# Performance work log

Hardware: AMD Instinct MI355X
Metric: run time of the kernel (lower is better)

Reference implementation:

```python
import jax, jax.numpy as jnp
import numpy as np

N_NODES = 50000
N_G_EDGES = 400000
N_LG_EDGES = 600000
N_HEADS = 4
OUT_FEATS = 64
EPS = 0.001


def segment_mean(x, seg_ids, num_segments):
    s = jax.ops.segment_sum(x, seg_ids, num_segments=num_segments)
    cnt = jax.ops.segment_sum(jnp.ones((x.shape[0],), x.dtype), seg_ids, num_segments=num_segments)
    return s / jnp.maximum(cnt, 1.0)[(...,) + (None,) * (x.ndim - 1)]


def setup_inputs() -> dict:
    key = jax.random.key(0)
    ks = jax.random.split(key, 12)
    return {
        'atomic_number': jax.random.randint(ks[0], (N_NODES,), 0, 4),
        'g_src': jax.random.randint(ks[1], (N_G_EDGES,), 0, N_NODES),
        'g_dst': jax.random.randint(ks[2], (N_G_EDGES,), 0, N_NODES),
        'lg_src': jax.random.randint(ks[3], (N_LG_EDGES,), 0, N_G_EDGES),
        'lg_dst': jax.random.randint(ks[4], (N_LG_EDGES,), 0, N_G_EDGES),
        'costheta': jax.random.uniform(ks[5], (N_LG_EDGES,), jnp.float32),
        'dnr': jax.random.uniform(ks[6], (N_LG_EDGES,), jnp.float32),
        'a': jax.random.uniform(ks[7], (N_HEADS,), jnp.float32),
        'b': jax.random.uniform(ks[8], (N_HEADS,), jnp.float32),
        'c': jax.random.uniform(ks[9], (N_HEADS,), jnp.float32),
        'd': jax.random.uniform(ks[10], (N_HEADS,), jnp.float32),
        'value_table': jax.random.normal(ks[11], (4, OUT_FEATS * N_HEADS), jnp.float32),
    }


def reference(atomic_number, g_src, g_dst, lg_src, lg_dst, costheta, dnr, a, b, c, d, value_table):
    # send_k_src: per g-edge atomic numbers of endpoints
    k_src = atomic_number[g_src]  # (E_g,)
    k_dst = atomic_number[g_dst]  # (E_g,)

    # masked symmetry key on line-graph edges (edge pair: lg_src -> lg_dst, g-edge indices)
    ka = k_src[lg_src]
    kc = k_dst[lg_dst]
    kb = k_dst[lg_src]
    peripheral = (ka == kc).astype(jnp.int32)
    central = ((kb == ka) & (kb == kc)).astype(jnp.int32)
    sym_key = peripheral * 2 + central  # (E_lg,), values in {0,1,2,3}

    # value embedding lookup -> (E_lg, F, H)
    asv = value_table[sym_key].reshape(N_LG_EDGES, OUT_FEATS, N_HEADS)

    # angular / radial symmetry per head
    ct = jnp.clip(costheta, -EPS, EPS)
    theta = jnp.arccos(ct)[:, None]  # (E_lg, 1)
    B = b % jnp.pi
    angular = ((jnp.cos(a[None, :] * theta + B[None, :]) + 1.0) / 2.0) ** c[None, :]  # (E_lg, H)
    radial = jnp.exp(-d[None, :] * (dnr[:, None] ** 2))  # (E_lg, H)
    spatial = radial * angular

    sv = asv * spatial[:, None, :]  # (E_lg, F, H)

    # reverse line-graph mean: aggregate lg edges by their (original) source lg-node = g-edge
    w_edge = segment_mean(sv, lg_src, N_G_EDGES)  # (E_g, F, H)
    # reverse graph mean: aggregate g edges by their (original) source node
    w_node = segment_mean(w_edge, g_src, N_NODES)  # (N, F, H)

    return jnp.sum(w_node, axis=-1)  # (N, F)
```

## Files before the change

### kernel.cpp

```cpp
#include <hip/hip_runtime.h>
#include <math.h>

typedef unsigned long long u64;
typedef unsigned int u32;
typedef unsigned short u16;
typedef unsigned char u8;

#define N_NODES    50000
#define N_G_EDGES  400000
#define N_LG_EDGES 600000
#define OUT_FEATS  64
#define EPSV       0.001f
#define PI_F       3.14159265358979323846f
#define HPI_F      1.57079632679489662f
#define FXSCALE    512.0f
#define INV_FXSCALE (1.0f/512.0f)

#define CT_SCALE   3.2e7f
#define CT_INV     (1.0f/3.2e7f)
#define DN_SCALE   65535.0f
#define DN_INV     (1.0f/65535.0f)

#define SB_N    256
#define EPB1    2344
#define GH_B0   256
#define GH_N    16
#define GH_EPC  25000
#define GH_W    12500
#define PK_B0   272
#define PK_GPB  3572
#define K1_GRID 384

#define WID   1564
#define NPB   196
#define SPB   (NPB*4)
#define CAP2  2816


__global__ __launch_bounds__(1024) void k1(const int* __restrict__ an,
                                           const int* __restrict__ gsrc,
                                           const int* __restrict__ gdst,
                                           const int* __restrict__ lgsrc,
                                           const int* __restrict__ lgdst,
                                           const float* __restrict__ costheta,
                                           const float* __restrict__ dnr,
                                           u8*  __restrict__ kk8,
                                           u32* __restrict__ cg,
                                           u32* __restrict__ prefT1,
                                           u64* __restrict__ sme64) {
    __shared__ u64 sm64[6250];
    const int tid = threadIdx.x;
    const int bid = blockIdx.x;

    if (bid < SB_N) {
        u64* metaS = sm64;
        u32* lcnt  = (u32*)(sm64 + 2344);
        u32* pref  = (u32*)(sm64 + 2344) + 256;
        if (tid < 256) lcnt[tid] = 0u;
        __syncthreads();

        const int e0 = bid * EPB1;
        const int e1 = (e0 + EPB1 < N_LG_EDGES) ? e0 + EPB1 : N_LG_EDGES;
        u64 pv[3]; u32 mv[3];
#pragma unroll
        for (int it = 0; it < 3; ++it) {
            mv[it] = 0u;
            int e = e0 + it * 1024 + tid;
            if (e < e1) {
                int ls = __builtin_nontemporal_load(&lgsrc[e]);
                int ld = __builtin_nontemporal_load(&lgdst[e]);
                float ct = __builtin_nontemporal_load(&costheta[e]);
                float dn = __builtin_nontemporal_load(&dnr[e]);
                float cc = fminf(fmaxf(ct, -EPSV), EPSV);
                u32 ct16 = (u32)(u16)(cc * CT_SCALE + 32768.0f + 0.5f);
                float dns = dn * DN_SCALE + 0.5f;
                u32 dn16 = (u32)(dns < 65535.0f ? (u16)dns : (u16)65535u);
                u32 bk = (u32)ls / WID;
                u32 li = (u32)ls - bk * WID;
                pv[it] = (u64)li | ((u64)(u32)ld << 11) | ((u64)dn16 << 30)
                       | ((u64)ct16 << 46);
                u32 rank = atomicAdd(&lcnt[bk], 1u);
                mv[it] = 0x80000000u | (rank << 8) | bk;
            }
        }
        __syncthreads();
        if (tid < 256) pref[tid + 1] = lcnt[tid];
        if (tid == 0) pref[0] = 0u;
        __syncthreads();
        for (int off = 1; off < 256; off <<= 1) {
            u32 add = 0;
            if (tid < 256 && tid >= off) add = pref[tid - off + 1];
            __syncthreads();
            if (tid < 256) pref[tid + 1] += add;
            __syncthreads();
        }
#pragma unroll
        for (int it = 0; it < 3; ++it) {
            if (mv[it] & 0x80000000u) {
                u32 bk = mv[it] & 0xffu;
                u32 pos = pref[bk] + ((mv[it] >> 8) & 0x7fffffu);
                metaS[pos] = pv[it];
            }
        }
        __syncthreads();
        const u32 btot = pref[256];
        for (u32 i = tid; i < btot; i += 1024)
            __builtin_nontemporal_store(metaS[i], &sme64[(size_t)bid * EPB1 + i]);
        if (tid <= 256) prefT1[bid * 257 + tid] = pref[tid];
    } else if (bid < PK_B0) {
        u32* hist = (u32*)sm64;
        const int cc = bid - GH_B0;
        for (int w = tid; w < GH_W; w += 1024) hist[w] = 0u;
        __syncthreads();
        const int s0 = cc * GH_EPC;
        for (int g = s0 + tid; g < s0 + GH_EPC; g += 1024) {
            int n = gsrc[g];
            atomicAdd(&hist[n >> 2], 1u << (8 * (n & 3)));
        }
        __syncthreads();
        for (int w = tid; w < GH_W; w += 1024) cg[cc * GH_W + w] = hist[w];
    } else {
        const int g0 = (bid - PK_B0) * PK_GPB;
        const int g1 = (g0 + PK_GPB < N_G_EDGES) ? g0 + PK_GPB : N_G_EDGES;
        for (int g = g0 + tid; g < g1; g += 1024)
            kk8[g] = (u8)(an[gsrc[g]] | (an[gdst[g]] << 4));
    }
}

__global__ __launch_bounds__(1024) void k2(const int* __restrict__ gsrc,
                                           const u8*  __restrict__ kk8,
                                           const u32* __restrict__ prefT1,
                                           const u64* __restrict__ sme64,
                                           const float* __restrict__ pa,
                                           const float* __restrict__ pb,
                                           const float* __restrict__ pc,
                                           const float* __restrict__ pd,
                                           u64* __restrict__ mq64,
                                           u32* __restrict__ prefT2) {
    __shared__ u64 sm64[5632 + 78];
    __shared__ u32 su[4154];
    u64* stage  = sm64;
    u64* outst  = sm64 + 2816;
    u32* cntinv = su;
    u32* nkw    = su + 1564;
    u32* sstart = su + 3128;
    u32* soff   = su + 3384;
    u32* lcnt2  = su + 3641;
    u32* pref2  = su + 3897;
    const int tid = threadIdx.x;
    const int b = blockIdx.x;
    const int lo = b * WID;

    for (int i = tid; i < WID; i += 1024) cntinv[i] = 0u;
    if (tid < 256) {
        u32 a = prefT1[tid * 257 + b];
        u32 c2 = prefT1[tid * 257 + b + 1];
        sstart[tid] = a; soff[tid + 1] = c2 - a; lcnt2[tid] = 0u;
    }
    if (tid == 0) soff[0] = 0u;
    __syncthreads();
    for (int off = 1; off < 256; off <<= 1) {
        u32 add = 0;
        if (tid < 256 && tid >= off) add = soff[tid - off + 1];
        __syncthreads();
        if (tid < 256) soff[tid + 1] += add;
        __syncthreads();
    }
    u32 total = soff[256]; if (total > CAP2) total = CAP2;

    {
        const int g = tid >> 2, lane = tid & 3;
        const u32 st = sstart[g];
        const u32 base = soff[g];
        const u32 len = soff[g + 1] - base;
        const u64* src = sme64 + (size_t)g * EPB1 + st;
        for (u32 j = lane; j < len; j += 4) {
            u32 p = base + j;
            if (p < CAP2) stage[p] = __builtin_nontemporal_load(&src[j]);
        }
    }
    for (int i = tid; i < WID; i += 1024) {
        int ls = lo + i;
        u32 nk = 0u;
        if (ls < N_G_EDGES)
            nk = (u32)(u16)gsrc[ls] | ((u32)kk8[ls] << 16);
        nkw[i] = nk;
    }
    __syncthreads();
    for (u32 i = tid; i < total; i += 1024)
        atomicAdd(&cntinv[(u32)(stage[i] & 0x7ffu)], 1u);
    __syncthreads();
    for (int i = tid; i < WID; i += 1024) {
        u32 c = cntinv[i];
        cntinv[i] = __float_as_uint(1.0f / (float)(c < 1u ? 1u : c));
    }
    __syncthreads();

    float A0[4], A1[4], A2[4], DD[4];
#pragma unroll
    for (int h = 0; h < 4; ++h) {
        float a = pa[h], B = fmodf(pb[h], PI_F), c = pc[h], d = pd[h];
        float K = a * HPI_F + B;
        float ck = cosf(K), sk = sinf(K);
        float u0 = 0.5f * (1.0f + ck);
        float f0 = powf(u0, c);
        float g1v = (-0.5f * a * sk) / u0;
        float u2 = -0.25f * a * a * ck;
        float g2v = u2 / u0 - 0.5f * g1v * g1v;
        A0[h] = f0;
        A1[h] = f0 * c * g1v;
        A2[h] = f0 * (c * g2v + 0.5f * c * c * g1v * g1v);
        DD[h] = d;
    }

    u64 qv[3]; u32 mv2[3];
#pragma unroll
    for (int it = 0; it < 3; ++it) {
        mv2[it] = 0u;
        u32 i = (u32)(it * 1024 + tid);
        if (i < total) {
            u64 v = stage[i];
            u32 li = (u32)(v & 0x7ffu);
            u32 ld = (u32)((v >> 11) & 0x7ffffu);
            float dn = (float)(u32)((v >> 30) & 0xffffu) * DN_INV;
            float ct = ((float)(u32)((v >> 46) & 0xffffu) - 32768.0f) * CT_INV;
            float inv = __uint_as_float(cntinv[li]);
            u32 nk = nkw[li];
            int node = (int)(nk & 0xffffu);
            u32 kw = (nk >> 16) & 0xffu;
            int ka = (int)(kw & 0xfu);
            int kb = (int)(kw >> 4);
            int kd = kk8[ld] >> 4;
            int key = ((ka == kd) ? 2 : 0) + ((kb == ka && kb == kd) ? 1 : 0);
            float del = -ct;
            float dn2 = dn * dn;
            float s = inv * FXSCALE;
            u64 q = 0;
#pragma unroll
            for (int h = 0; h < 4; ++h) {
                float ang = A0[h] + del * (A1[h] + del * A2[h]);
                float rad = __expf(-DD[h] * dn2);
                q |= (u64)(u32)(ang * rad * s + 0.5f) << (10 * h);
            }
            u32 nb = (u32)node / NPB;
            u32 slot = ((u32)node - nb * NPB) * 4u + (u32)key;
            u32 rank = atomicAdd(&lcnt2[nb], 1u);
            qv[it] = (q << 10) | (u64)slot;
            mv2[it] = 0x80000000u | (rank << 18) | (nb << 10);
        }
    }
    __syncthreads();
    if (tid < 256) pref2[tid + 1] = lcnt2[tid];
    if (tid == 0) pref2[0] = 0u;
    __syncthreads();
    for (int off = 1; off < 256; off <<= 1) {
        u32 add = 0;
        if (tid < 256 && tid >= off) add = pref2[tid - off + 1];
        __syncthreads();
        if (tid < 256) pref2[tid + 1] += add;
        __syncthreads();
    }
#pragma unroll
    for (int it = 0; it < 3; ++it) {
        if (mv2[it] & 0x80000000u) {
            u32 nb = (mv2[it] >> 10) & 0xffu;
            u32 pos = pref2[nb] + ((mv2[it] >> 18) & 0x1fffu);
            if (pos < CAP2) outst[pos] = qv[it];
        }
    }
    __syncthreads();
    u32 t2 = pref2[256]; if (t2 > CAP2) t2 = CAP2;
    for (u32 i = tid; i < t2; i += 1024)
        __builtin_nontemporal_store(outst[i], &mq64[(size_t)b * CAP2 + i]);
    if (tid <= 256) {
        u32 v = pref2[tid];
        prefT2[b * 257 + tid] = (v < CAP2) ? v : CAP2;
    }
}

__global__ __launch_bounds__(1024) void k3(const u64* __restrict__ mq64,
                                           const u32* __restrict__ prefT2,
                                           const u32* __restrict__ cg,
                                           const float* __restrict__ VT,
                                           float* __restrict__ out) {
    __shared__ u64 sm64[2816 + 784];
    __shared__ u32 su[2506];
    u64* stage  = sm64;
    u64* ts     = sm64 + 2816;
    float* vt_s = (float*)su;
    float* ivg  = (float*)(su + 1024);
    u32* sstart = su + 1220;
    u32* soff   = su + 1476;
    const int tid = threadIdx.x;
    const int nb = blockIdx.x;

    for (int i = tid; i < SPB; i += 1024) ts[i] = 0ull;
    vt_s[tid] = VT[tid];
    if (tid < NPB) {
        int n = nb * NPB + tid;
        float iv = 0.0f;
        if (n < N_NODES) {
            int w = n >> 2, sh = 8 * (n & 3);
            u32 c = 0;
#pragma unroll
            for (int cc = 0; cc < GH_N; ++cc)
                c += (cg[cc * GH_W + w] >> sh) & 0xffu;
            iv = 1.0f / (float)(c < 1u ? 1u : c);
        }
        ivg[tid] = iv;
    }
    if (tid < 256) {
        u32 a = prefT2[tid * 257 + nb];
        u32 c2 = prefT2[tid * 257 + nb + 1];
        sstart[tid] = a; soff[tid + 1] = c2 - a;
    }
    if (tid == 0) soff[0] = 0u;
    __syncthreads();
    for (int off = 1; off < 256; off <<= 1) {
        u32 add = 0;
        if (tid < 256 && tid >= off) add = soff[tid - off + 1];
        __syncthreads();
        if (tid < 256) soff[tid + 1] += add;
        __syncthreads();
    }
    u32 total = soff[256]; if (total > CAP2) total = CAP2;

    {
        const int g = tid >> 2, lane = tid & 3;
        const u32 st = sstart[g];
        const u32 base = soff[g];
        const u32 len = soff[g + 1] - base;
        const u64* src = mq64 + (size_t)g * CAP2 + st;
        for (u32 j = lane; j < len; j += 4) {
            u32 p = base + j;
            if (p < CAP2) stage[p] = __builtin_nontemporal_load(&src[j]);
        }
    }
    __syncthreads();

    for (u32 i = tid; i < total; i += 1024) {
        u64 v = stage[i];
        u32 slot = (u32)(v & 0x3ffu);
        u64 q = ((v >> 10) & 0x3ffu) | (((v >> 20) & 0x3ffu) << 16)
              | (((v >> 30) & 0x3ffu) << 32) | (((v >> 40) & 0x3ffu) << 48);
        atomicAdd(&ts[slot], q);
    }
    __syncthreads();

    const int n0 = nb * NPB;
    for (int j = tid; j < NPB * OUT_FEATS; j += 1024) {
        int nl = j >> 6, f = j & 63;
        int n = n0 + nl;
        if (n < N_NODES) {
            float acc = 0.0f;
#pragma unroll
            for (int k = 0; k < 4; ++k) {
                u64 t = ts[nl * 4 + k];
#pragma unroll
                for (int h = 0; h < 4; ++h) {
                    float tv = (float)((u32)(t >> (16 * h)) & 0xffffu);
                    acc += vt_s[k * 256 + f * 4 + h] * tv;
                }
            }
            __builtin_nontemporal_store(acc * INV_FXSCALE * ivg[nl],
                                        &out[n * OUT_FEATS + f]);
        }
    }
}

extern "C" void kernel_launch(void* const* d_in, const int* in_sizes, int n_in,
                              void* d_out, int out_size, void* d_ws, size_t ws_size,
                              hipStream_t stream) {
    const int*   an       = (const int*)d_in[0];
    const int*   gsrc     = (const int*)d_in[1];
    const int*   gdst     = (const int*)d_in[2];
    const int*   lgsrc    = (const int*)d_in[3];
    const int*   lgdst    = (const int*)d_in[4];
    const float* costheta = (const float*)d_in[5];
    const float* dnr      = (const float*)d_in[6];
    const float* pa       = (const float*)d_in[7];
    const float* pb       = (const float*)d_in[8];
    const float* pc       = (const float*)d_in[9];
    const float* pd       = (const float*)d_in[10];
    const float* vt       = (const float*)d_in[11];
    float* out = (float*)d_out;

    char* ws = (char*)d_ws;
    u8*  kk8    = (u8*) (ws + 0);
    u32* cg     = (u32*)(ws + 400000);
    u32* prefT1 = (u32*)(ws + 1200000);
    u32* prefT2 = (u32*)(ws + 1463168);
    u64* sme64  = (u64*)(ws + 1726336);
    u64* mq64   = (u64*)(ws + 6526848);

    k1<<<dim3(K1_GRID), dim3(1024), 0, stream>>>(
        an, gsrc, gdst, lgsrc, lgdst, costheta, dnr, kk8, cg, prefT1, sme64);
    k2<<<dim3(256), dim3(1024), 0, stream>>>(
        gsrc, kk8, prefT1, sme64, pa, pb, pc, pd, mq64, prefT2);
    k3<<<dim3(256), dim3(1024), 0, stream>>>(
        mq64, prefT2, cg, vt, out);
}
```

Before: 48.51 us.

## Double bucket count to 512 blocks of 512 threads across all three kernels

Re-partitions the three-pass bucketed scatter/reduce pipeline from 256 blocks of 1024 threads to 512 blocks of 512 threads. Bucket widths, capacities and the bit-packing layouts shrink to match. The source-node histogram is also split into range-restricted sub-blocks so each fits in smaller shared memory. The aim is more blocks to fill the 256 CUs and less shared memory per block. In exchange, each block does a longer 512-step prefix scan, the gather loop becomes one serial thread per source segment, and the prefix tables are larger.

```diff
diff --git a/kernel.cpp b/kernel.cpp
--- a/kernel.cpp
+++ b/kernel.cpp
@@ -21,51 +21,54 @@
 #define DN_SCALE   65535.0f
 #define DN_INV     (1.0f/65535.0f)
 
-#define SB_N    256
-#define EPB1    2344
-#define GH_B0   256
-#define GH_N    16
+#define NB    512
+#define NTH   512
+#define WID   782
+#define EPB   1172
+#define CAP3  1536
+#define NPB   98
+#define SPB   (NPB*4)
+
+#define GH_B0   512
+#define GH_CH   16
 #define GH_EPC  25000
-#define GH_W    12500
-#define PK_B0   272
+#define GH_BR   3125
+#define GH_W    782
+#define GH_CSTR 12512
+#define PK_B0   768
 #define PK_GPB  3572
-#define K1_GRID 384
-
-#define WID   1564
-#define NPB   196
-#define SPB   (NPB*4)
-#define CAP2  2816
-
-
-__global__ __launch_bounds__(1024) void k1(const int* __restrict__ an,
-                                           const int* __restrict__ gsrc,
-                                           const int* __restrict__ gdst,
-                                           const int* __restrict__ lgsrc,
-                                           const int* __restrict__ lgdst,
-                                           const float* __restrict__ costheta,
-                                           const float* __restrict__ dnr,
-                                           u8*  __restrict__ kk8,
-                                           u32* __restrict__ cg,
-                                           u32* __restrict__ prefT1,
-                                           u64* __restrict__ sme64) {
-    __shared__ u64 sm64[6250];
+#define K1_GRID 880
+
+
+__global__ __launch_bounds__(NTH) void k1(const int* __restrict__ an,
+                                          const int* __restrict__ gsrc,
+                                          const int* __restrict__ gdst,
+                                          const int* __restrict__ lgsrc,
+                                          const int* __restrict__ lgdst,
+                                          const float* __restrict__ costheta,
+                                          const float* __restrict__ dnr,
+                                          u8*  __restrict__ kk8,
+                                          u32* __restrict__ cg,
+                                          u32* __restrict__ prefT1,
+                                          u64* __restrict__ sme64) {
+    __shared__ u64 stageS[EPB];
+    __shared__ u32 su[1025];
     const int tid = threadIdx.x;
     const int bid = blockIdx.x;
 
-    if (bid < SB_N) {
-        u64* metaS = sm64;
-        u32* lcnt  = (u32*)(sm64 + 2344);
-        u32* pref  = (u32*)(sm64 + 2344) + 256;
-        if (tid < 256) lcnt[tid] = 0u;
-        __syncthreads();
-
-        const int e0 = bid * EPB1;
-        const int e1 = (e0 + EPB1 < N_LG_EDGES) ? e0 + EPB1 : N_LG_EDGES;
+    if (bid < NB) {
+        u32* lcnt = su;
+        u32* pref = su + 512;
+        lcnt[tid] = 0u;
+        __syncthreads();
+
+        const int e0 = bid * EPB;
+        const int e1 = (e0 + EPB < N_LG_EDGES) ? e0 + EPB : N_LG_EDGES;
         u64 pv[3]; u32 mv[3];
 #pragma unroll
         for (int it = 0; it < 3; ++it) {
             mv[it] = 0u;
-            int e = e0 + it * 1024 + tid;
+            int e = e0 + it * NTH + tid;
             if (e < e1) {
                 int ls = __builtin_nontemporal_load(&lgsrc[e]);
                 int ld = __builtin_nontemporal_load(&lgdst[e]);
@@ -77,109 +80,111 @@
                 u32 dn16 = (u32)(dns < 65535.0f ? (u16)dns : (u16)65535u);
                 u32 bk = (u32)ls / WID;
                 u32 li = (u32)ls - bk * WID;
-                pv[it] = (u64)li | ((u64)(u32)ld << 11) | ((u64)dn16 << 30)
-                       | ((u64)ct16 << 46);
+                pv[it] = (u64)li | ((u64)(u32)ld << 10) | ((u64)dn16 << 29)
+                       | ((u64)ct16 << 45);
                 u32 rank = atomicAdd(&lcnt[bk], 1u);
-                mv[it] = 0x80000000u | (rank << 8) | bk;
+                mv[it] = 0x80000000u | (rank << 19) | (bk << 10);
             }
         }
         __syncthreads();
-        if (tid < 256) pref[tid + 1] = lcnt[tid];
+        pref[tid + 1] = lcnt[tid];
         if (tid == 0) pref[0] = 0u;
         __syncthreads();
-        for (int off = 1; off < 256; off <<= 1) {
+        for (int off = 1; off < NB; off <<= 1) {
             u32 add = 0;
-            if (tid < 256 && tid >= off) add = pref[tid - off + 1];
+            if (tid >= off) add = pref[tid - off + 1];
             __syncthreads();
-            if (tid < 256) pref[tid + 1] += add;
+            pref[tid + 1] += add;
             __syncthreads();
         }
 #pragma unroll
         for (int it = 0; it < 3; ++it) {
             if (mv[it] & 0x80000000u) {
-                u32 bk = mv[it] & 0xffu;
-                u32 pos = pref[bk] + ((mv[it] >> 8) & 0x7fffffu);
-                metaS[pos] = pv[it];
+                u32 bk = (mv[it] >> 10) & 0x1ffu;
+                u32 pos = pref[bk] + ((mv[it] >> 19) & 0x7ffu);
+                stageS[pos] = pv[it];
             }
         }
         __syncthreads();
-        const u32 btot = pref[256];
-        for (u32 i = tid; i < btot; i += 1024)
-            __builtin_nontemporal_store(metaS[i], &sme64[(size_t)bid * EPB1 + i]);
-        if (tid <= 256) prefT1[bid * 257 + tid] = pref[tid];
+        const u32 btot = pref[NB];
+        for (u32 i = tid; i < btot; i += NTH)
+            __builtin_nontemporal_store(stageS[i], &sme64[(size_t)bid * EPB + i]);
+        prefT1[bid * 513 + tid] = pref[tid];
+        if (tid == 0) prefT1[bid * 513 + 512] = pref[512];
     } else if (bid < PK_B0) {
-        u32* hist = (u32*)sm64;
-        const int cc = bid - GH_B0;
-        for (int w = tid; w < GH_W; w += 1024) hist[w] = 0u;
+        u32* hist = su;
+        const int b2 = bid - GH_B0;
+        const int cc = b2 & 15, r = b2 >> 4;
+        const int lo = r * GH_BR;
+        for (int w = tid; w < GH_W; w += NTH) hist[w] = 0u;
         __syncthreads();
         const int s0 = cc * GH_EPC;
-        for (int g = s0 + tid; g < s0 + GH_EPC; g += 1024) {
-            int n = gsrc[g];
-            atomicAdd(&hist[n >> 2], 1u << (8 * (n & 3)));
-        }
-        __syncthreads();
-        for (int w = tid; w < GH_W; w += 1024) cg[cc * GH_W + w] = hist[w];
+        for (int g = s0 + tid; g < s0 + GH_EPC; g += NTH) {
+            unsigned lb = (unsigned)(gsrc[g] - lo);
+            if (lb < (unsigned)GH_BR)
+                atomicAdd(&hist[lb >> 2], 1u << (8 * (lb & 3)));
+        }
+        __syncthreads();
+        for (int w = tid; w < GH_W; w += NTH)
+            cg[cc * GH_CSTR + r * GH_W + w] = hist[w];
     } else {
         const int g0 = (bid - PK_B0) * PK_GPB;
         const int g1 = (g0 + PK_GPB < N_G_EDGES) ? g0 + PK_GPB : N_G_EDGES;
-        for (int g = g0 + tid; g < g1; g += 1024)
+        for (int g = g0 + tid; g < g1; g += NTH)
             kk8[g] = (u8)(an[gsrc[g]] | (an[gdst[g]] << 4));
     }
 }
 
-__global__ __launch_bounds__(1024) void k2(const int* __restrict__ gsrc,
-                                           const u8*  __restrict__ kk8,
-                                           const u32* __restrict__ prefT1,
-                                           const u64* __restrict__ sme64,
-                                           const float* __restrict__ pa,
-                                           const float* __restrict__ pb,
-                                           const float* __restrict__ pc,
-                                           const float* __restrict__ pd,
-                                           u64* __restrict__ mq64,
-                                           u32* __restrict__ prefT2) {
-    __shared__ u64 sm64[5632 + 78];
-    __shared__ u32 su[4154];
-    u64* stage  = sm64;
-    u64* outst  = sm64 + 2816;
-    u32* cntinv = su;
-    u32* nkw    = su + 1564;
-    u32* sstart = su + 3128;
-    u32* soff   = su + 3384;
-    u32* lcnt2  = su + 3641;
-    u32* pref2  = su + 3897;
+__global__ __launch_bounds__(NTH) void k2(const int* __restrict__ gsrc,
+                                          const u8*  __restrict__ kk8,
+                                          const u32* __restrict__ prefT1,
+                                          const u64* __restrict__ sme64,
+                                          const float* __restrict__ pa,
+                                          const float* __restrict__ pb,
+                                          const float* __restrict__ pc,
+                                          const float* __restrict__ pd,
+                                          u64* __restrict__ mq64,
+                                          u32* __restrict__ prefT2) {
+    __shared__ u64 stage[CAP3];
+    __shared__ u64 outst[CAP3];
+    __shared__ u32 cntinv[WID];
+    __shared__ u32 nkw[WID];
+    __shared__ u32 sstart[NB];
+    __shared__ u32 soff[NB + 1];
+    __shared__ u32 lcnt2[NB];
+    __shared__ u32 pref2[NB + 1];
     const int tid = threadIdx.x;
     const int b = blockIdx.x;
     const int lo = b * WID;
 
-    for (int i = tid; i < WID; i += 1024) cntinv[i] = 0u;
-    if (tid < 256) {
-        u32 a = prefT1[tid * 257 + b];
-        u32 c2 = prefT1[tid * 257 + b + 1];
+    for (int i = tid; i < WID; i += NTH) cntinv[i] = 0u;
+    {
+        u32 a = prefT1[tid * 513 + b];
+        u32 c2 = prefT1[tid * 513 + b + 1];
         sstart[tid] = a; soff[tid + 1] = c2 - a; lcnt2[tid] = 0u;
     }
     if (tid == 0) soff[0] = 0u;
     __syncthreads();
-    for (int off = 1; off < 256; off <<= 1) {
+    for (int off = 1; off < NB; off <<= 1) {
         u32 add = 0;
-        if (tid < 256 && tid >= off) add = soff[tid - off + 1];
-        __syncthreads();
-        if (tid < 256) soff[tid + 1] += add;
-        __syncthreads();
-    }
-    u32 total = soff[256]; if (total > CAP2) total = CAP2;
+        if (tid >= off) add = soff[tid - off + 1];
+        __syncthreads();
+        soff[tid + 1] += add;
+        __syncthreads();
+    }
+    u32 total = soff[NB]; if (total > CAP3) total = CAP3;
 
     {
-        const int g = tid >> 2, lane = tid & 3;
-        const u32 st = sstart[g];
-        const u32 base = soff[g];
-        const u32 len = soff[g + 1] - base;
-        const u64* src = sme64 + (size_t)g * EPB1 + st;
-        for (u32 j = lane; j < len; j += 4) {
+        const u32 st = sstart[tid];
+        const u32 base = soff[tid];
+        const u32 len = soff[tid + 1] - base;
+        const u64* src = sme64 + (size_t)tid * EPB + st;
+        for (u32 j = 0; j < len; ++j) {
             u32 p = base + j;
-            if (p < CAP2) stage[p] = __builtin_nontemporal_load(&src[j]);
-        }
-    }
-    for (int i = tid; i < WID; i += 1024) {
+            if (p < CAP3) stage[p] = __builtin_nontemporal_load(&src[j]);
+        }
+    }
+    for (int i = tid; i < WID; i += NTH) {
         int ls = lo + i;
         u32 nk = 0u;
         if (ls < N_G_EDGES)
@@ -187,10 +192,10 @@
         nkw[i] = nk;
     }
     __syncthreads();
-    for (u32 i = tid; i < total; i += 1024)
-        atomicAdd(&cntinv[(u32)(stage[i] & 0x7ffu)], 1u);
-    __syncthreads();
-    for (int i = tid; i < WID; i += 1024) {
+    for (u32 i = tid; i < total; i += NTH)
+        atomicAdd(&cntinv[(u32)(stage[i] & 0x3ffu)], 1u);
+    __syncthreads();
+    for (int i = tid; i < WID; i += NTH) {
         u32 c = cntinv[i];
         cntinv[i] = __float_as_uint(1.0f / (float)(c < 1u ? 1u : c));
     }
@@ -217,13 +222,13 @@
 #pragma unroll
     for (int it = 0; it < 3; ++it) {
         mv2[it] = 0u;
-        u32 i = (u32)(it * 1024 + tid);
+        u32 i = (u32)(it * NTH + tid);
         if (i < total) {
             u64 v = stage[i];
-            u32 li = (u32)(v & 0x7ffu);
-            u32 ld = (u32)((v >> 11) & 0x7ffffu);
-            float dn = (float)(u32)((v >> 30) & 0xffffu) * DN_INV;
-            float ct = ((float)(u32)((v >> 46) & 0xffffu) - 32768.0f) * CT_INV;
+            u32 li = (u32)(v & 0x3ffu);
+            u32 ld = (u32)((v >> 10) & 0x7ffffu);
+            float dn = (float)(u32)((v >> 29) & 0xffffu) * DN_INV;
+            float ct = ((float)(u32)((v >> 45) & 0xffffu) - 32768.0f) * CT_INV;
             float inv = __uint_as_float(cntinv[li]);
             u32 nk = nkw[li];
             int node = (int)(nk & 0xffffu);
@@ -246,99 +251,102 @@
             u32 slot = ((u32)node - nb * NPB) * 4u + (u32)key;
             u32 rank = atomicAdd(&lcnt2[nb], 1u);
             qv[it] = (q << 10) | (u64)slot;
-            mv2[it] = 0x80000000u | (rank << 18) | (nb << 10);
-        }
-    }
-    __syncthreads();
-    if (tid < 256) pref2[tid + 1] = lcnt2[tid];
+            mv2[it] = 0x80000000u | (rank << 19) | (nb << 10);
+        }
+    }
+    __syncthreads();
+    pref2[tid + 1] = lcnt2[tid];
     if (tid == 0) pref2[0] = 0u;
     __syncthreads();
-    for (int off = 1; off < 256; off <<= 1) {
+    for (int off = 1; off < NB; off <<= 1) {
         u32 add = 0;
-        if (tid < 256 && tid >= off) add = pref2[tid - off + 1];
-        __syncthreads();
-        if (tid < 256) pref2[tid + 1] += add;
+        if (tid >= off) add = pref2[tid - off + 1];
+        __syncthreads();
+        pref2[tid + 1] += add;
         __syncthreads();
     }
 #pragma unroll
     for (int it = 0; it < 3; ++it) {
         if (mv2[it] & 0x80000000u) {
-            u32 nb = (mv2[it] >> 10) & 0xffu;
-            u32 pos = pref2[nb] + ((mv2[it] >> 18) & 0x1fffu);
-            if (pos < CAP2) outst[pos] = qv[it];
-        }
-    }
-    __syncthreads();
-    u32 t2 = pref2[256]; if (t2 > CAP2) t2 = CAP2;
-    for (u32 i = tid; i < t2; i += 1024)
-        __builtin_nontemporal_store(outst[i], &mq64[(size_t)b * CAP2 + i]);
-    if (tid <= 256) {
+            u32 nb = (mv2[it] >> 10) & 0x1ffu;
+            u32 pos = pref2[nb] + ((mv2[it] >> 19) & 0x7ffu);
+            if (pos < CAP3) outst[pos] = qv[it];
+        }
+    }
+    __syncthreads();
+    u32 t2 = pref2[NB]; if (t2 > CAP3) t2 = CAP3;
+    for (u32 i = tid; i < t2; i += NTH)
+        __builtin_nontemporal_store(outst[i], &mq64[(size_t)b * CAP3 + i]);
+    {
         u32 v = pref2[tid];
-        prefT2[b * 257 + tid] = (v < CAP2) ? v : CAP2;
+        prefT2[b * 513 + tid] = (v < CAP3) ? v : CAP3;
+    }
+    if (tid == 0) {
+        u32 v = pref2[512];
+        prefT2[b * 513 + 512] = (v < CAP3) ? v : CAP3;
     }
 }
 
-__global__ __launch_bounds__(1024) void k3(const u64* __restrict__ mq64,
-                                           const u32* __restrict__ prefT2,
-                                           const u32* __restrict__ cg,
-                                           const float* __restrict__ VT,
-                                           float* __restrict__ out) {
-    __shared__ u64 sm64[2816 + 784];
-    __shared__ u32 su[2506];
-    u64* stage  = sm64;
-    u64* ts     = sm64 + 2816;
-    float* vt_s = (float*)su;
-    float* ivg  = (float*)(su + 1024);
-    u32* sstart = su + 1220;
-    u32* soff   = su + 1476;
+__global__ __launch_bounds__(NTH) void k3(const u64* __restrict__ mq64,
+                                          const u32* __restrict__ prefT2,
+                                          const u32* __restrict__ cg,
+                                          const float* __restrict__ VT,
+                                          float* __restrict__ out) {
+    __shared__ u64 stage[CAP3];
+    __shared__ u64 ts[SPB];
+    __shared__ float vt_s[1024];
+    __shared__ float ivg[NPB];
+    __shared__ u32 sstart[NB];
+    __shared__ u32 soff[NB + 1];
     const int tid = threadIdx.x;
     const int nb = blockIdx.x;
 
-    for (int i = tid; i < SPB; i += 1024) ts[i] = 0ull;
+    for (int i = tid; i < SPB; i += NTH) ts[i] = 0ull;
     vt_s[tid] = VT[tid];
+    vt_s[tid + 512] = VT[tid + 512];
     if (tid < NPB) {
         int n = nb * NPB + tid;
         float iv = 0.0f;
         if (n < N_NODES) {
-            int w = n >> 2, sh = 8 * (n & 3);
+            int r = n / GH_BR, lb = n - r * GH_BR;
+            int w = lb >> 2, sh = 8 * (lb & 3);
             u32 c = 0;
 #pragma unroll
-            for (int cc = 0; cc < GH_N; ++cc)
-                c += (cg[cc * GH_W + w] >> sh) & 0xffu;
+            for (int cc = 0; cc < GH_CH; ++cc)
+                c += (cg[cc * GH_CSTR + r * GH_W + w] >> sh) & 0xffu;
             iv = 1.0f / (float)(c < 1u ? 1u : c);
         }
         ivg[tid] = iv;
     }
-    if (tid < 256) {
-        u32 a = prefT2[tid * 257 + nb];
-        u32 c2 = prefT2[tid * 257 + nb + 1];
+    {
+        u32 a = prefT2[tid * 513 + nb];
+        u32 c2 = prefT2[tid * 513 + nb + 1];
         sstart[tid] = a; soff[tid + 1] = c2 - a;
     }
     if (tid == 0) soff[0] = 0u;
     __syncthreads();
-    for (int off = 1; off < 256; off <<= 1) {
+    for (int off = 1; off < NB; off <<= 1) {
         u32 add = 0;
-        if (tid < 256 && tid >= off) add = soff[tid - off + 1];
-        __syncthreads();
-        if (tid < 256) soff[tid + 1] += add;
-        __syncthreads();
-    }
-    u32 total = soff[256]; if (total > CAP2) total = CAP2;
+        if (tid >= off) add = soff[tid - off + 1];
+        __syncthreads();
+        soff[tid + 1] += add;
+        __syncthreads();
+    }
+    u32 total = soff[NB]; if (total > CAP3) total = CAP3;
 
     {
-        const int g = tid >> 2, lane = tid & 3;
-        const u32 st = sstart[g];
-        const u32 base = soff[g];
-        const u32 len = soff[g + 1] - base;
-        const u64* src = mq64 + (size_t)g * CAP2 + st;
-        for (u32 j = lane; j < len; j += 4) {
+        const u32 st = sstart[tid];
+        const u32 base = soff[tid];
+        const u32 len = soff[tid + 1] - base;
+        const u64* src = mq64 + (size_t)tid * CAP3 + st;
+        for (u32 j = 0; j < len; ++j) {
             u32 p = base + j;
-            if (p < CAP2) stage[p] = __builtin_nontemporal_load(&src[j]);
-        }
-    }
-    __syncthreads();
-
-    for (u32 i = tid; i < total; i += 1024) {
+            if (p < CAP3) stage[p] = __builtin_nontemporal_load(&src[j]);
+        }
+    }
+    __syncthreads();
+
+    for (u32 i = tid; i < total; i += NTH) {
         u64 v = stage[i];
         u32 slot = (u32)(v & 0x3ffu);
         u64 q = ((v >> 10) & 0x3ffu) | (((v >> 20) & 0x3ffu) << 16)
@@ -348,7 +356,7 @@
     __syncthreads();
 
     const int n0 = nb * NPB;
-    for (int j = tid; j < NPB * OUT_FEATS; j += 1024) {
+    for (int j = tid; j < NPB * OUT_FEATS; j += NTH) {
         int nl = j >> 6, f = j & 63;
         int n = n0 + nl;
         if (n < N_NODES) {
@@ -388,15 +396,15 @@
     char* ws = (char*)d_ws;
     u8*  kk8    = (u8*) (ws + 0);
     u32* cg     = (u32*)(ws + 400000);
-    u32* prefT1 = (u32*)(ws + 1200000);
-    u32* prefT2 = (u32*)(ws + 1463168);
-    u64* sme64  = (u64*)(ws + 1726336);
-    u64* mq64   = (u64*)(ws + 6526848);
-
-    k1<<<dim3(K1_GRID), dim3(1024), 0, stream>>>(
+    u32* prefT1 = (u32*)(ws + 1200768);
+    u32* prefT2 = (u32*)(ws + 2251392);
+    u64* sme64  = (u64*)(ws + 3302016);
+    u64* mq64   = (u64*)(ws + 8102528);
+
+    k1<<<dim3(K1_GRID), dim3(NTH), 0, stream>>>(
         an, gsrc, gdst, lgsrc, lgdst, costheta, dnr, kk8, cg, prefT1, sme64);
-    k2<<<dim3(256), dim3(1024), 0, stream>>>(
+    k2<<<dim3(NB), dim3(NTH), 0, stream>>>(
         gsrc, kk8, prefT1, sme64, pa, pb, pc, pd, mq64, prefT2);
-    k3<<<dim3(256), dim3(1024), 0, stream>>>(
+    k3<<<dim3(NB), dim3(NTH), 0, stream>>>(
         mq64, prefT2, cg, vt, out);
 }
```

Measured after the change: 74.69 us. 54.0% more time.
